# Kernel optimization log

Measured on AMD Instinct MI355X. Metric: run time of the kernel, lower is better.

The kernel has to match this reference:

```python
import jax, jax.numpy as jnp
import numpy as np

B, C, H, W = 4, 3, 32, 32
N_IMAGES = 32
TIMESTEPS = 20


def _extract_patches(x, pad_mode):
    """3x3 patches at every spatial location. x: [B,C,H,W] -> [B,C,9,H,W]."""
    if pad_mode == 'wrap':
        xp = jnp.pad(x, ((0, 0), (0, 0), (1, 1), (1, 1)), mode='wrap')
    else:
        xp = jnp.pad(x, ((0, 0), (0, 0), (1, 1), (1, 1)))
    h, w = x.shape[2], x.shape[3]
    sl = [xp[:, :, di:di + h, dj:dj + w] for di in range(3) for dj in range(3)]
    return jnp.stack(sl, axis=2)  # [B,C,9,H,W], k = di*3+dj (torch unfold order)


def setup_inputs() -> dict:
    key = jax.random.key(0)
    k1, k2 = jax.random.split(key)
    x = jax.random.normal(k1, (B, C, H, W), dtype=jnp.float32)
    images = jax.random.uniform(k2, (N_IMAGES, C, H, W), dtype=jnp.float32)
    # linear beta schedule, as in _noise_buffers
    betas = jnp.linspace(1e-4, 0.02, TIMESTEPS, dtype=jnp.float32)
    alpha_cumprod = jnp.cumprod(1.0 - betas)
    mu_sched = jnp.sqrt(alpha_cumprod)
    sigma_sched = jnp.sqrt(1.0 - alpha_cumprod)
    return {"x": x, "images": images, "mu_sched": mu_sched,
            "sigma_sched": sigma_sched, "t": 10}


def reference(x, images, mu_sched, sigma_sched, t):
    mu = mu_sched[t]
    sigma = sigma_sched[t]
    b, c, h, w = x.shape

    # x-side: circular-padded 3x3 patches and their squared norms
    xp = _extract_patches(x, 'wrap').reshape(b, c * 9, h, w)   # [B,C*9,H,W]
    x_norms = jnp.sum(xp * xp, axis=1)                          # [B,H,W]

    # dataset-side: zero-padded 3x3 patches at every pixel of every image
    ip = _extract_patches(images, 'zeros')                      # [N,C,9,H,W]
    patches = ip.transpose(0, 3, 4, 1, 2).reshape(-1, c * 9)    # [P, C*9], P=N*H*W
    pnorms = jnp.sum(patches * patches, axis=1)                 # [P]
    pcenters = patches.reshape(-1, c, 9)[:, :, 4]               # [P,C] center pixel (1,1)

    # conv2d(x_pad, patches) == contraction over the C*9 patch axis
    conv = jnp.einsum('bkhw,pk->bphw', xp, patches)             # [B,P,H,W]

    inv2s2 = 1.0 / (2.0 * sigma * sigma)
    log_w = -(x_norms[:, None] - 2.0 * mu * conv
              + (mu * mu) * pnorms[None, :, None, None]) * inv2s2  # [B,P,H,W]

    # stable softmax-style weights over the patch axis (== online LSE result)
    m = jnp.max(log_w, axis=1)                                  # [B,H,W]
    wgt = jnp.exp(log_w - m[:, None])                           # [B,P,H,W]
    sum_w = jnp.sum(wgt, axis=1)                                # [B,H,W]

    # sum_p w * (x - mu * pcenter) = x*sum_w - mu * (w @ pcenters)
    wc = jnp.einsum('bphw,pc->bchw', wgt, pcenters)             # [B,C,H,W]
    sum_wd = x * sum_w[:, None] - mu * wc
    return -sum_wd / (sigma * sigma * sum_w[:, None])
```

## Files before the change

kernel.cpp:

```cpp
#include <hip/hip_runtime.h>
#include <cstddef>

#define P_TOTAL 32768
#define Q_TOTAL 4096
#define NSPLIT 64
#define KPS 512
#define TILES 32
#define QPERWG 256
#define NQG (Q_TOTAL / QPERWG)
#define GRID (NSPLIT * NQG)

typedef _Float16 half8 __attribute__((ext_vector_type(8)));
typedef float floatx4 __attribute__((ext_vector_type(4)));

__device__ __forceinline__ float fexp2(float x) {
#if defined(__has_builtin) && __has_builtin(__builtin_amdgcn_exp2f)
    return __builtin_amdgcn_exp2f(x);
#else
    return exp2f(x);
#endif
}

__global__ __launch_bounds__(256) void qbuild_k(
    const float* __restrict__ x, _Float16* __restrict__ q16)
{
    int q = blockIdx.x * 256 + threadIdx.x;
    int b = q >> 10, rem = q & 1023, h = rem >> 5, w = rem & 31;
    const float* xb = x + (size_t)b * 3072;
    _Float16 row[32];
    #pragma unroll
    for (int c = 0; c < 3; c++)
      #pragma unroll
      for (int di = 0; di < 3; di++)
        #pragma unroll
        for (int dj = 0; dj < 3; dj++)
            row[c * 9 + di * 3 + dj] =
                (_Float16)xb[c * 1024 + ((h + di + 31) & 31) * 32 + ((w + dj + 31) & 31)];
    row[27] = (_Float16)1.0f;
    row[28] = (_Float16)0.f; row[29] = (_Float16)0.f;
    row[30] = (_Float16)0.f; row[31] = (_Float16)0.f;
    _Float16* qp = q16 + (size_t)q * 32;
    #pragma unroll
    for (int u = 0; u < 4; u++) ((float4*)qp)[u] = ((float4*)row)[u];
}

__global__ __launch_bounds__(256) void score_k(
    const _Float16* __restrict__ q16, const float* __restrict__ images,
    const float* __restrict__ mu_sched, const float* __restrict__ sigma_sched,
    const int* __restrict__ tptr, float* __restrict__ partials)
{
    __shared__ char lds[KPS * 64 + KPS * 8];
    _Float16* ctr16 = (_Float16*)(lds + KPS * 64);
    int tid = threadIdx.x;
    int split = blockIdx.x >> 4;
    int qg    = blockIdx.x & 15;

    int t = tptr[0];
    float mu = mu_sched[t], sg = sigma_sched[t];
    const float LOG2E = 1.4426950408889634f;
    float inv2s2 = 1.0f / (2.0f * sg * sg);
    float s1     = 2.0f * mu * inv2s2 * LOG2E;
    float bscale = -mu * mu * inv2s2 * LOG2E;

    #pragma unroll
    for (int kk = 0; kk < 2; kk++) {
        int r = tid + kk * 256;
        int p = split * KPS + r;
        int n = p >> 10, rem = p & 1023, i = rem >> 5, j = rem & 31;
        const float* img = images + (size_t)n * 3072;
        _Float16 hrow[32];
        float pnorm = 0.f, c0 = 0.f, c1 = 0.f, c2 = 0.f;
        #pragma unroll
        for (int c = 0; c < 3; c++)
          #pragma unroll
          for (int di = 0; di < 3; di++)
            #pragma unroll
            for (int dj = 0; dj < 3; dj++) {
                int ii = i + di - 1, jj = j + dj - 1;
                float val = 0.f;
                if (ii >= 0 && ii < 32 && jj >= 0 && jj < 32)
                    val = img[c * 1024 + ii * 32 + jj];
                hrow[c * 9 + di * 3 + dj] = (_Float16)(val * s1);
                pnorm = fmaf(val, val, pnorm);
                if (di == 1 && dj == 1) { if (c == 0) c0 = val; else if (c == 1) c1 = val; else c2 = val; }
            }
        hrow[27] = (_Float16)(pnorm * bscale);
        hrow[28] = (_Float16)0.f; hrow[29] = (_Float16)0.f;
        hrow[30] = (_Float16)0.f; hrow[31] = (_Float16)0.f;
        int sw = (r >> 1) & 3;
        float4* src4 = (float4*)hrow;
        #pragma unroll
        for (int c = 0; c < 4; c++)
            *(float4*)(lds + r * 64 + ((c ^ sw) << 4)) = src4[c];
        _Float16 crow[4] = {(_Float16)c0, (_Float16)c1, (_Float16)c2, (_Float16)0.f};
        *(float2*)(ctr16 + (size_t)r * 4) = *(float2*)crow;
    }

    int lane = tid & 63, wid = tid >> 6;
    int col  = lane & 15, quad = lane >> 4;
    int qbase = qg * QPERWG + wid * 64;

    half8 qf[4];
    #pragma unroll
    for (int f = 0; f < 4; f++)
        qf[f] = *(const half8*)(q16 + (size_t)(qbase + f * 16 + col) * 32 + quad * 8);
    __syncthreads();

    int swc = (col >> 1) & 3;
    const char* abase = lds + col * 64 + ((quad ^ swc) << 4);

    float mx[4] = {-3e38f, -3e38f, -3e38f, -3e38f};
    {
        #pragma unroll 4
        for (int tile = 0; tile < TILES; tile++) {
            half8 ak = *(const half8*)(abase + tile * 1024);
            #pragma unroll
            for (int f = 0; f < 4; f++) {
                floatx4 a = __builtin_amdgcn_mfma_f32_16x16x32_f16(
                    ak, qf[f], (floatx4){0.f, 0.f, 0.f, 0.f}, 0, 0, 0);
                mx[f] = fmaxf(mx[f], fmaxf(fmaxf(a[0], a[1]), fmaxf(a[2], a[3])));
            }
        }
    }
    #pragma unroll
    for (int f = 0; f < 4; f++) {
        mx[f] = fmaxf(mx[f], __shfl_xor(mx[f], 16, 64));
        mx[f] = fmaxf(mx[f], __shfl_xor(mx[f], 32, 64));
    }
    floatx4 nmv[4];
    #pragma unroll
    for (int f = 0; f < 4; f++)
        nmv[f] = (floatx4){-mx[f], -mx[f], -mx[f], -mx[f]};

    float sv[4] = {0.f, 0.f, 0.f, 0.f};
    float w0[4] = {0.f, 0.f, 0.f, 0.f};
    float w1[4] = {0.f, 0.f, 0.f, 0.f};
    float w2[4] = {0.f, 0.f, 0.f, 0.f};
    {
        #pragma unroll 2
        for (int tile = 0; tile < TILES; tile++) {
            half8 ak = *(const half8*)(abase + tile * 1024);
            int gr = tile * 16 + quad * 4;
            half8 chA = *(const half8*)(ctr16 + (size_t)gr * 4);
            half8 chB = *(const half8*)(ctr16 + (size_t)(gr + 2) * 4);
            float c0v[4] = {(float)chA[0], (float)chA[4], (float)chB[0], (float)chB[4]};
            float c1v[4] = {(float)chA[1], (float)chA[5], (float)chB[1], (float)chB[5]};
            float c2v[4] = {(float)chA[2], (float)chA[6], (float)chB[2], (float)chB[6]};
            #pragma unroll
            for (int f = 0; f < 4; f++) {
                floatx4 a = __builtin_amdgcn_mfma_f32_16x16x32_f16(ak, qf[f], nmv[f], 0, 0, 0);
                #pragma unroll
                for (int r = 0; r < 4; r++) {
                    float e = fexp2(a[r]);
                    sv[f] += e;
                    w0[f] = fmaf(e, c0v[r], w0[f]);
                    w1[f] = fmaf(e, c1v[r], w1[f]);
                    w2[f] = fmaf(e, c2v[r], w2[f]);
                }
            }
        }
    }
    #pragma unroll
    for (int f = 0; f < 4; f++) {
        sv[f] += __shfl_xor(sv[f], 16, 64);  sv[f] += __shfl_xor(sv[f], 32, 64);
        w0[f] += __shfl_xor(w0[f], 16, 64);  w0[f] += __shfl_xor(w0[f], 32, 64);
        w1[f] += __shfl_xor(w1[f], 16, 64);  w1[f] += __shfl_xor(w1[f], 32, 64);
        w2[f] += __shfl_xor(w2[f], 16, 64);  w2[f] += __shfl_xor(w2[f], 32, 64);
    }

    if (quad == 0) {
        #pragma unroll
        for (int f = 0; f < 4; f++) {
            int q = qbase + f * 16 + col;
            float* pp = partials + ((size_t)split * Q_TOTAL + q) * 8;
            *(float4*)pp = make_float4(mx[f], sv[f], w0[f], w1[f]);
            pp[4] = w2[f];
        }
    }
}

__global__ __launch_bounds__(256) void combine_k(
    const float* __restrict__ x, const float* __restrict__ partials,
    const float* __restrict__ mu_sched, const float* __restrict__ sigma_sched,
    const int* __restrict__ tptr, float* __restrict__ out)
{
    int q = blockIdx.x * 256 + threadIdx.x;
    int t = tptr[0];
    float mu = mu_sched[t], sg = sigma_sched[t];
    float inv_s2 = 1.0f / (sg * sg);

    float M = -3e38f, S = 0.f, W0 = 0.f, W1 = 0.f, W2 = 0.f;
    for (int sp = 0; sp < NSPLIT; sp++) {
        const float* pp = partials + ((size_t)sp * Q_TOTAL + q) * 8;
        float4 a = *(const float4*)pp;
        float w2v = pp[4];
        float mnew = fmaxf(M, a.x);
        float sco = fexp2(M - mnew);
        float scn = fexp2(a.x - mnew);
        S  = fmaf(S,  sco, a.y * scn);
        W0 = fmaf(W0, sco, a.z * scn);
        W1 = fmaf(W1, sco, a.w * scn);
        W2 = fmaf(W2, sco, w2v * scn);
        M = mnew;
    }
    float invS = 1.0f / S;
    int b = q >> 10, rem = q & 1023;
    #pragma unroll
    for (int c = 0; c < 3; c++) {
        float Wc = (c == 0) ? W0 : (c == 1 ? W1 : W2);
        float xc = x[(size_t)b * 3072 + c * 1024 + rem];
        out[(size_t)b * 3072 + c * 1024 + rem] = -(xc - mu * Wc * invS) * inv_s2;
    }
}

extern "C" void kernel_launch(void* const* d_in, const int* in_sizes, int n_in,
                              void* d_out, int out_size, void* d_ws, size_t ws_size,
                              hipStream_t stream) {
    const float* x      = (const float*)d_in[0];
    const float* images = (const float*)d_in[1];
    const float* mu_s   = (const float*)d_in[2];
    const float* sg_s   = (const float*)d_in[3];
    const int*   tptr   = (const int*)d_in[4];
    float* out = (float*)d_out;

    float*    partials = (float*)d_ws;
    _Float16* q16      = (_Float16*)((char*)d_ws + (size_t)NSPLIT * Q_TOTAL * 8 * 4);

    qbuild_k<<<Q_TOTAL / 256, 256, 0, stream>>>(x, q16);
    score_k<<<GRID, 256, 0, stream>>>(q16, images, mu_s, sg_s, tptr, partials);
    combine_k<<<Q_TOTAL / 256, 256, 0, stream>>>(
        x, partials, mu_s, sg_s, tptr, out);
}
```

Measured before the change: 113.4 us.

## Double split count, store centers in fp32 SoA, pack math as float2, SoA partials

Halves keys per workgroup and doubles the number of splits, which doubles the grid for more parallelism and shortens each workgroup's serial loops. Patch center pixels are now stored in LDS as fp32 structure-of-arrays instead of packed fp16, so the inner loop no longer needs the half-to-float conversions. Max, sum and weighted-center accumulations are rewritten on float2 vectors so the compiler can emit packed fp32 ops. Partials are written as separate planes so the combine kernel's loads coalesce. The trade-off is more redundant patch building across workgroups and twice as many partials for the combine kernel to merge serially.

```diff
diff --git a/kernel.cpp b/kernel.cpp
--- a/kernel.cpp
+++ b/kernel.cpp
@@ -3,15 +3,16 @@
 
 #define P_TOTAL 32768
 #define Q_TOTAL 4096
-#define NSPLIT 64
-#define KPS 512
-#define TILES 32
+#define NSPLIT 128
+#define KPS 256
+#define TILES 16
 #define QPERWG 256
 #define NQG (Q_TOTAL / QPERWG)
 #define GRID (NSPLIT * NQG)
 
 typedef _Float16 half8 __attribute__((ext_vector_type(8)));
 typedef float floatx4 __attribute__((ext_vector_type(4)));
+typedef float floatx2 __attribute__((ext_vector_type(2)));
 
 __device__ __forceinline__ float fexp2(float x) {
 #if defined(__has_builtin) && __has_builtin(__builtin_amdgcn_exp2f)
@@ -49,8 +50,8 @@
     const float* __restrict__ mu_sched, const float* __restrict__ sigma_sched,
     const int* __restrict__ tptr, float* __restrict__ partials)
 {
-    __shared__ char lds[KPS * 64 + KPS * 8];
-    _Float16* ctr16 = (_Float16*)(lds + KPS * 64);
+    __shared__ char lds[KPS * 64 + 3 * KPS * 4];
+    float* ctrp = (float*)(lds + KPS * 64);
     int tid = threadIdx.x;
     int split = blockIdx.x >> 4;
     int qg    = blockIdx.x & 15;
@@ -62,9 +63,8 @@
     float s1     = 2.0f * mu * inv2s2 * LOG2E;
     float bscale = -mu * mu * inv2s2 * LOG2E;
 
-    #pragma unroll
-    for (int kk = 0; kk < 2; kk++) {
-        int r = tid + kk * 256;
+    {
+        int r = tid;
         int p = split * KPS + r;
         int n = p >> 10, rem = p & 1023, i = rem >> 5, j = rem & 31;
         const float* img = images + (size_t)n * 3072;
@@ -92,8 +92,9 @@
         #pragma unroll
         for (int c = 0; c < 4; c++)
             *(float4*)(lds + r * 64 + ((c ^ sw) << 4)) = src4[c];
-        _Float16 crow[4] = {(_Float16)c0, (_Float16)c1, (_Float16)c2, (_Float16)0.f};
-        *(float2*)(ctr16 + (size_t)r * 4) = *(float2*)crow;
+        ctrp[0 * KPS + r] = c0;
+        ctrp[1 * KPS + r] = c1;
+        ctrp[2 * KPS + r] = c2;
     }
 
     int lane = tid & 63, wid = tid >> 6;
@@ -109,7 +110,9 @@
     int swc = (col >> 1) & 3;
     const char* abase = lds + col * 64 + ((quad ^ swc) << 4);
 
-    float mx[4] = {-3e38f, -3e38f, -3e38f, -3e38f};
+    floatx2 mx2[4];
+    #pragma unroll
+    for (int f = 0; f < 4; f++) mx2[f] = (floatx2){-3e38f, -3e38f};
     {
         #pragma unroll 4
         for (int tile = 0; tile < TILES; tile++) {
@@ -118,12 +121,17 @@
             for (int f = 0; f < 4; f++) {
                 floatx4 a = __builtin_amdgcn_mfma_f32_16x16x32_f16(
                     ak, qf[f], (floatx4){0.f, 0.f, 0.f, 0.f}, 0, 0, 0);
-                mx[f] = fmaxf(mx[f], fmaxf(fmaxf(a[0], a[1]), fmaxf(a[2], a[3])));
+                floatx2 alo = __builtin_shufflevector(a, a, 0, 1);
+                floatx2 ahi = __builtin_shufflevector(a, a, 2, 3);
+                mx2[f] = __builtin_elementwise_max(
+                    mx2[f], __builtin_elementwise_max(alo, ahi));
             }
         }
     }
+    float mx[4];
     #pragma unroll
     for (int f = 0; f < 4; f++) {
+        mx[f] = fmaxf(mx2[f].x, mx2[f].y);
         mx[f] = fmaxf(mx[f], __shfl_xor(mx[f], 16, 64));
         mx[f] = fmaxf(mx[f], __shfl_xor(mx[f], 32, 64));
     }
@@ -132,49 +140,59 @@
     for (int f = 0; f < 4; f++)
         nmv[f] = (floatx4){-mx[f], -mx[f], -mx[f], -mx[f]};
 
-    float sv[4] = {0.f, 0.f, 0.f, 0.f};
-    float w0[4] = {0.f, 0.f, 0.f, 0.f};
-    float w1[4] = {0.f, 0.f, 0.f, 0.f};
-    float w2[4] = {0.f, 0.f, 0.f, 0.f};
+    floatx2 sv2[4], w02[4], w12[4], w22[4];
+    #pragma unroll
+    for (int f = 0; f < 4; f++) {
+        sv2[f] = (floatx2){0.f, 0.f};
+        w02[f] = sv2[f]; w12[f] = sv2[f]; w22[f] = sv2[f];
+    }
     {
         #pragma unroll 2
         for (int tile = 0; tile < TILES; tile++) {
             half8 ak = *(const half8*)(abase + tile * 1024);
             int gr = tile * 16 + quad * 4;
-            half8 chA = *(const half8*)(ctr16 + (size_t)gr * 4);
-            half8 chB = *(const half8*)(ctr16 + (size_t)(gr + 2) * 4);
-            float c0v[4] = {(float)chA[0], (float)chA[4], (float)chB[0], (float)chB[4]};
-            float c1v[4] = {(float)chA[1], (float)chA[5], (float)chB[1], (float)chB[5]};
-            float c2v[4] = {(float)chA[2], (float)chA[6], (float)chB[2], (float)chB[6]};
+            floatx4 c0q = *(const floatx4*)(ctrp + 0 * KPS + gr);
+            floatx4 c1q = *(const floatx4*)(ctrp + 1 * KPS + gr);
+            floatx4 c2q = *(const floatx4*)(ctrp + 2 * KPS + gr);
+            floatx2 c0a = __builtin_shufflevector(c0q, c0q, 0, 1);
+            floatx2 c0b = __builtin_shufflevector(c0q, c0q, 2, 3);
+            floatx2 c1a = __builtin_shufflevector(c1q, c1q, 0, 1);
+            floatx2 c1b = __builtin_shufflevector(c1q, c1q, 2, 3);
+            floatx2 c2a = __builtin_shufflevector(c2q, c2q, 0, 1);
+            floatx2 c2b = __builtin_shufflevector(c2q, c2q, 2, 3);
             #pragma unroll
             for (int f = 0; f < 4; f++) {
                 floatx4 a = __builtin_amdgcn_mfma_f32_16x16x32_f16(ak, qf[f], nmv[f], 0, 0, 0);
-                #pragma unroll
-                for (int r = 0; r < 4; r++) {
-                    float e = fexp2(a[r]);
-                    sv[f] += e;
-                    w0[f] = fmaf(e, c0v[r], w0[f]);
-                    w1[f] = fmaf(e, c1v[r], w1[f]);
-                    w2[f] = fmaf(e, c2v[r], w2[f]);
-                }
+                floatx2 e01 = {fexp2(a[0]), fexp2(a[1])};
+                floatx2 e23 = {fexp2(a[2]), fexp2(a[3])};
+                sv2[f] += e01 + e23;
+                w02[f] = __builtin_elementwise_fma(e01, c0a, w02[f]);
+                w02[f] = __builtin_elementwise_fma(e23, c0b, w02[f]);
+                w12[f] = __builtin_elementwise_fma(e01, c1a, w12[f]);
+                w12[f] = __builtin_elementwise_fma(e23, c1b, w12[f]);
+                w22[f] = __builtin_elementwise_fma(e01, c2a, w22[f]);
+                w22[f] = __builtin_elementwise_fma(e23, c2b, w22[f]);
             }
         }
     }
+
     #pragma unroll
     for (int f = 0; f < 4; f++) {
-        sv[f] += __shfl_xor(sv[f], 16, 64);  sv[f] += __shfl_xor(sv[f], 32, 64);
-        w0[f] += __shfl_xor(w0[f], 16, 64);  w0[f] += __shfl_xor(w0[f], 32, 64);
-        w1[f] += __shfl_xor(w1[f], 16, 64);  w1[f] += __shfl_xor(w1[f], 32, 64);
-        w2[f] += __shfl_xor(w2[f], 16, 64);  w2[f] += __shfl_xor(w2[f], 32, 64);
-    }
-
-    if (quad == 0) {
-        #pragma unroll
-        for (int f = 0; f < 4; f++) {
-            int q = qbase + f * 16 + col;
-            float* pp = partials + ((size_t)split * Q_TOTAL + q) * 8;
-            *(float4*)pp = make_float4(mx[f], sv[f], w0[f], w1[f]);
-            pp[4] = w2[f];
+        float sv = sv2[f].x + sv2[f].y;
+        float w0 = w02[f].x + w02[f].y;
+        float w1 = w12[f].x + w12[f].y;
+        float w2 = w22[f].x + w22[f].y;
+        sv += __shfl_xor(sv, 16, 64);  sv += __shfl_xor(sv, 32, 64);
+        w0 += __shfl_xor(w0, 16, 64);  w0 += __shfl_xor(w0, 32, 64);
+        w1 += __shfl_xor(w1, 16, 64);  w1 += __shfl_xor(w1, 32, 64);
+        w2 += __shfl_xor(w2, 16, 64);  w2 += __shfl_xor(w2, 32, 64);
+        if (quad == 0) {
+            size_t idx = (size_t)split * Q_TOTAL + qbase + f * 16 + col;
+            partials[idx]                          = mx[f];
+            partials[idx + (size_t)NSPLIT * Q_TOTAL]     = sv;
+            partials[idx + (size_t)NSPLIT * Q_TOTAL * 2] = w0;
+            partials[idx + (size_t)NSPLIT * Q_TOTAL * 3] = w1;
+            partials[idx + (size_t)NSPLIT * Q_TOTAL * 4] = w2;
         }
     }
 }
@@ -189,17 +207,21 @@
     float mu = mu_sched[t], sg = sigma_sched[t];
     float inv_s2 = 1.0f / (sg * sg);
 
+    const size_t PL = (size_t)NSPLIT * Q_TOTAL;
     float M = -3e38f, S = 0.f, W0 = 0.f, W1 = 0.f, W2 = 0.f;
     for (int sp = 0; sp < NSPLIT; sp++) {
-        const float* pp = partials + ((size_t)sp * Q_TOTAL + q) * 8;
-        float4 a = *(const float4*)pp;
-        float w2v = pp[4];
-        float mnew = fmaxf(M, a.x);
+        size_t idx = (size_t)sp * Q_TOTAL + q;
+        float mval = partials[idx];
+        float sval = partials[idx + PL];
+        float w0v  = partials[idx + PL * 2];
+        float w1v  = partials[idx + PL * 3];
+        float w2v  = partials[idx + PL * 4];
+        float mnew = fmaxf(M, mval);
         float sco = fexp2(M - mnew);
-        float scn = fexp2(a.x - mnew);
-        S  = fmaf(S,  sco, a.y * scn);
-        W0 = fmaf(W0, sco, a.z * scn);
-        W1 = fmaf(W1, sco, a.w * scn);
+        float scn = fexp2(mval - mnew);
+        S  = fmaf(S,  sco, sval * scn);
+        W0 = fmaf(W0, sco, w0v * scn);
+        W1 = fmaf(W1, sco, w1v * scn);
         W2 = fmaf(W2, sco, w2v * scn);
         M = mnew;
     }
@@ -224,7 +246,7 @@
     float* out = (float*)d_out;
 
     float*    partials = (float*)d_ws;
-    _Float16* q16      = (_Float16*)((char*)d_ws + (size_t)NSPLIT * Q_TOTAL * 8 * 4);
+    _Float16* q16      = (_Float16*)((char*)d_ws + (size_t)5 * NSPLIT * Q_TOTAL * 4);
 
     qbuild_k<<<Q_TOTAL / 256, 256, 0, stream>>>(x, q16);
     score_k<<<GRID, 256, 0, stream>>>(q16, images, mu_s, sg_s, tptr, partials);
```

Result: slower. 120.7 us (+6.4%).
